# Performance work log

Measured on AMD Instinct MI355X. Metric: run time of the kernel, lower is better.

## Reference

```python
import jax, jax.numpy as jnp
import numpy as np

B, D, K, P = 512, 2048, 128, 5

def setup_inputs() -> dict:
    key = jax.random.key(0)
    k1, k2 = jax.random.split(key)
    x = jax.random.normal(k1, (B, D), dtype=jnp.float32)
    theta = 0.05 * jax.random.normal(k2, (D, K, P), dtype=jnp.float32)
    log_weight_scale = jnp.zeros((K, P), dtype=jnp.float32)
    bias = -jnp.ones((K,), dtype=jnp.float32)  # layer inits bias to -1
    return {"x": x, "theta": theta, "log_weight_scale": log_weight_scale, "bias": bias}

def reference(x, theta, log_weight_scale, bias):
    b = x.shape[0]
    # weight-normalized kernel: [D, K, P]
    norm = jnp.sqrt(jnp.sum(theta * theta, axis=0))            # [K, P]
    kernel = theta * (jnp.exp(log_weight_scale) / norm)[None]  # [D, K, P]
    actv = jnp.einsum('bd,dkp->bkp', x, kernel)                # [B, K, P]
    # pairwise L1 over P: [B, K, B]
    diff = jnp.abs(actv[:, :, :, None] - jnp.transpose(actv, (1, 2, 0))[None])  # [B,K,P,B]
    abs_dif = jnp.sum(diff, axis=2) + 1e6 * jnp.eye(b, dtype=x.dtype)[:, None, :]
    f = jnp.sum(jnp.exp(-abs_dif), axis=2) + bias[None, :]     # [B, K]
    return jnp.concatenate([x, f], axis=1)                     # [B, D+K]
```

## Files before the change

kernel.cpp:

```cpp
#include <hip/hip_runtime.h>
#include <math.h>

#define BSZ 512
#define DD 2048
#define KK 128
#define PP 5
#define NCOL (KK * PP)
#define OUTW (DD + KK)
#define LOG2E 1.4426950408889634f

#define KSPLIT 8
#define GK (DD / KSPLIT)
#define QSPLIT 8

typedef __attribute__((ext_vector_type(8))) short bf16x8;
typedef __attribute__((ext_vector_type(4))) float f32x4;

#define WS_NORM 0
#define WS_ACTV (WS_NORM + NCOL)
#define WS_FPART (WS_ACTV + BSZ * NCOL)
#define WS_XB (WS_FPART + QSPLIT * KK * BSZ)
#define WS_THT (WS_XB + BSZ * DD / 2)
#define WS_PART (WS_THT + NCOL * DD / 2)

__device__ inline ushort f2b(float f) {
    unsigned u = __float_as_uint(f);
    u += 0x7FFF + ((u >> 16) & 1);
    return (ushort)(u >> 16);
}

__global__ __launch_bounds__(256) void prep_kernel(const float* __restrict__ theta,
                                                   const float* __restrict__ x,
                                                   float* __restrict__ norm,
                                                   ushort* __restrict__ thT,
                                                   ushort* __restrict__ xb) {
    __shared__ float partial[32][8];
    __shared__ ushort sT[64][68];

    const int bid = blockIdx.x;
    const int t   = threadIdx.x;

    if (bid < 80) {
        const int c8  = bid * 8;
        const int col = c8 + (t & 7);
        const int g   = t >> 3;
        const float* p = theta + (size_t)g * NCOL + col;
        float s = 0.f;
#pragma unroll
        for (int j = 0; j < 64; ++j) {
            float v = p[(size_t)j * 32 * NCOL];
            s += v * v;
        }
        partial[g][t & 7] = s;
        __syncthreads();
        if (t < 8) {
            float acc = 0.f;
#pragma unroll
            for (int gg = 0; gg < 32; ++gg) acc += partial[gg][t];
            norm[c8 + t] = acc;
        }
    } else if (bid < 400) {
        const int tb    = bid - 80;
        const int kz    = (tb & 31) * 64;
        const int nz    = (tb >> 5) * 64;
        const int c4    = t & 15;
        const int rbase = t >> 4;
#pragma unroll
        for (int i = 0; i < 4; ++i) {
            int r = rbase + i * 16;
            float4 v = *(const float4*)&theta[(size_t)(kz + r) * NCOL + nz + c4 * 4];
            sT[c4 * 4 + 0][r] = f2b(v.x);
            sT[c4 * 4 + 1][r] = f2b(v.y);
            sT[c4 * 4 + 2][r] = f2b(v.z);
            sT[c4 * 4 + 3][r] = f2b(v.w);
        }
        __syncthreads();
#pragma unroll
        for (int i = 0; i < 2; ++i) {
            int slot = t + i * 256;
            int rr   = slot >> 3;
            int cc   = (slot & 7) * 8;
            ushort4 w0 = *(const ushort4*)&sT[rr][cc];
            ushort4 w1 = *(const ushort4*)&sT[rr][cc + 4];
            ushort* dst = &thT[(size_t)(nz + rr) * DD + kz + cc];
            *(ushort4*)&dst[0] = w0;
            *(ushort4*)&dst[4] = w1;
        }
    } else {
        const int b2 = bid - 400;
#pragma unroll
        for (int i = 0; i < 4; ++i) {
            int base = b2 * 4096 + i * 1024 + t * 4;
            float4 v = *(const float4*)&x[base];
            ushort4 w;
            w.x = f2b(v.x); w.y = f2b(v.y); w.z = f2b(v.z); w.w = f2b(v.w);
            *(ushort4*)&xb[base] = w;
        }
    }
}

__global__ __launch_bounds__(256) void gemm_kernel(const ushort* __restrict__ xb,
                                                   const ushort* __restrict__ thT,
                                                   float* __restrict__ part,
                                                   const float* __restrict__ x,
                                                   float* __restrict__ out) {
    __shared__ ushort lA[64][136];
    __shared__ ushort lB[64][136];

    if (blockIdx.z == KSPLIT) {
        const int bid = blockIdx.y * 10 + blockIdx.x;
        for (int i = bid * 256 + threadIdx.x; i < BSZ * (DD / 4); i += 80 * 256) {
            int r = i >> 9;
            int c = i & 511;
            float4 v = *(const float4*)&x[(size_t)r * DD + c * 4];
            *(float4*)&out[(size_t)r * OUTW + c * 4] = v;
        }
        return;
    }

    const int t    = threadIdx.x;
    const int lane = t & 63;
    const int wave = t >> 6;
    const int bn   = blockIdx.x * 64;
    const int bm   = blockIdx.y * 64;
    const int kz   = blockIdx.z * GK;

    const ushort* gA = xb  + (size_t)bm * DD + kz;
    const ushort* gB = thT + (size_t)bn * DD + kz;

    f32x4 acc[2][2] = {};

    uint4 va[4], vb[4];
#pragma unroll
    for (int i = 0; i < 4; ++i) {
        int slot = t + i * 256, rr = slot >> 4, ss = slot & 15;
        va[i] = *(const uint4*)&gA[(size_t)rr * DD + ss * 8];
        vb[i] = *(const uint4*)&gB[(size_t)rr * DD + ss * 8];
    }

    const int fr = lane & 15;
    const int g  = lane >> 4;
    const int mr = (wave >> 1) * 32 + fr;
    const int nr = (wave & 1) * 32 + fr;

#pragma unroll
    for (int c = 0; c < 2; ++c) {
        __syncthreads();
#pragma unroll
        for (int i = 0; i < 4; ++i) {
            int slot = t + i * 256, rr = slot >> 4, ss = slot & 15;
            *(uint4*)&lA[rr][ss * 8] = va[i];
            *(uint4*)&lB[rr][ss * 8] = vb[i];
        }
        __syncthreads();
        if (c == 0) {
#pragma unroll
            for (int i = 0; i < 4; ++i) {
                int slot = t + i * 256, rr = slot >> 4, ss = slot & 15;
                va[i] = *(const uint4*)&gA[(size_t)rr * DD + 128 + ss * 8];
                vb[i] = *(const uint4*)&gB[(size_t)rr * DD + 128 + ss * 8];
            }
        }
#pragma unroll
        for (int ks = 0; ks < 4; ++ks) {
            const int kc = ks * 32 + g * 8;
            bf16x8 a0 = *(const bf16x8*)&lA[mr][kc];
            bf16x8 a1 = *(const bf16x8*)&lA[mr + 16][kc];
            bf16x8 b0 = *(const bf16x8*)&lB[nr][kc];
            bf16x8 b1 = *(const bf16x8*)&lB[nr + 16][kc];
            acc[0][0] = __builtin_amdgcn_mfma_f32_16x16x32_bf16(a0, b0, acc[0][0], 0, 0, 0);
            acc[0][1] = __builtin_amdgcn_mfma_f32_16x16x32_bf16(a0, b1, acc[0][1], 0, 0, 0);
            acc[1][0] = __builtin_amdgcn_mfma_f32_16x16x32_bf16(a1, b0, acc[1][0], 0, 0, 0);
            acc[1][1] = __builtin_amdgcn_mfma_f32_16x16x32_bf16(a1, b1, acc[1][1], 0, 0, 0);
        }
    }

    float* base = part + (size_t)blockIdx.z * (BSZ * NCOL);
#pragma unroll
    for (int mt = 0; mt < 2; ++mt)
#pragma unroll
        for (int nt = 0; nt < 2; ++nt) {
            int row = bm + (wave >> 1) * 32 + mt * 16 + g * 4;
            int col = bn + (wave & 1) * 32 + nt * 16 + fr;
            float* dst = base + (size_t)row * NCOL + col;
#pragma unroll
            for (int reg = 0; reg < 4; ++reg)
                dst[(size_t)reg * NCOL] = acc[mt][nt][reg];
        }
}

__global__ __launch_bounds__(256) void reduce_kernel(const float* __restrict__ part,
                                                     const float* __restrict__ norm,
                                                     const float* __restrict__ lws,
                                                     float* __restrict__ actv) {
    int i   = blockIdx.x * 256 + threadIdx.x;
    int col = i % NCOL;
    float s = 0.f;
#pragma unroll
    for (int q = 0; q < KSPLIT; ++q)
        s += part[(size_t)q * (BSZ * NCOL) + i];
    const float scale = __builtin_amdgcn_exp2f(lws[col] * LOG2E) *
                        __builtin_amdgcn_rsqf(norm[col]) * LOG2E;
    actv[i] = s * scale;
}

__global__ __launch_bounds__(256) void pairwise_kernel(const float* __restrict__ actv,
                                                       float* __restrict__ f_part) {
    const int k   = blockIdx.x;
    const int q   = blockIdx.y;
    const int tid = threadIdx.x;

    __shared__ float sB[64][8];

    for (int i = tid; i < 64 * PP; i += 256) {
        int r = i / PP;
        int p = i - r * PP;
        sB[r][p] = actv[(size_t)(q * 64 + r) * NCOL + k * PP + p];
    }

    float a[2][PP];
#pragma unroll
    for (int r = 0; r < 2; ++r) {
        const float* ap = &actv[(size_t)(tid + r * 256) * NCOL + k * PP];
#pragma unroll
        for (int p = 0; p < PP; ++p) a[r][p] = ap[p];
    }
    __syncthreads();

    float acc[2] = {0.f, 0.f};
#pragma unroll 4
    for (int j = 0; j < 64; ++j) {
        const float4 v  = *(const float4*)&sB[j][0];
        const float  v4 = sB[j][4];
#pragma unroll
        for (int r = 0; r < 2; ++r) {
            float s = fabsf(a[r][0] - v.x) + fabsf(a[r][1] - v.y) +
                      fabsf(a[r][2] - v.z) + fabsf(a[r][3] - v.w) +
                      fabsf(a[r][4] - v4);
            acc[r] += __builtin_amdgcn_exp2f(-s);
        }
    }

    float* fp = f_part + ((size_t)q * KK + k) * BSZ;
    fp[tid]       = acc[0];
    fp[tid + 256] = acc[1];
}

__global__ __launch_bounds__(256) void freduce_kernel(const float* __restrict__ f_part,
                                                      const float* __restrict__ bias,
                                                      float* __restrict__ out) {
    int i = blockIdx.x * 256 + threadIdx.x;
    int k = i >> 9;
    int b = i & 511;
    float s = 0.f;
#pragma unroll
    for (int q = 0; q < QSPLIT; ++q)
        s += f_part[((size_t)q * KK + k) * BSZ + b];
    out[(size_t)b * OUTW + DD + k] = s - 1.0f + bias[k];
}

extern "C" void kernel_launch(void* const* d_in, const int* in_sizes, int n_in,
                              void* d_out, int out_size, void* d_ws, size_t ws_size,
                              hipStream_t stream) {
    const float* x     = (const float*)d_in[0];
    const float* theta = (const float*)d_in[1];
    const float* lws   = (const float*)d_in[2];
    const float* bias  = (const float*)d_in[3];
    float* out = (float*)d_out;

    float* ws     = (float*)d_ws;
    float* norm   = ws + WS_NORM;
    float* actv   = ws + WS_ACTV;
    float* f_part = ws + WS_FPART;
    ushort* xb    = (ushort*)(ws + WS_XB);
    ushort* thT   = (ushort*)(ws + WS_THT);
    float* part   = ws + WS_PART;

    prep_kernel<<<656, 256, 0, stream>>>(theta, x, norm, thT, xb);
    gemm_kernel<<<dim3(NCOL / 64, BSZ / 64, KSPLIT + 1), 256, 0, stream>>>(xb, thT, part, x, out);
    reduce_kernel<<<(BSZ * NCOL) / 256, 256, 0, stream>>>(part, norm, lws, actv);
    pairwise_kernel<<<dim3(KK, QSPLIT), 256, 0, stream>>>(actv, f_part);
    freduce_kernel<<<256, 256, 0, stream>>>(f_part, bias, out);
}
```

Before: 117.8 us.

## Drop split-K in GEMM, fuse scaling epilogue, swizzle LDS tiles

The GEMM no longer splits K eight ways. Each of 80 blocks now loops over the full K=2048 in 16 chunks and writes the scaled activations directly, so the partial-sum buffer and the separate reduce kernel go away. The LDS tiles switch from padded rows to an XOR-swizzled layout to avoid bank conflicts. This saves a launch and the large partial read/write traffic, but leaves only 80 GEMM blocks on a many-CU GPU, each with a longer serial K loop, which may underutilize the device.

```diff
diff --git a/kernel.cpp b/kernel.cpp
--- a/kernel.cpp
+++ b/kernel.cpp
@@ -9,8 +9,6 @@
 #define OUTW (DD + KK)
 #define LOG2E 1.4426950408889634f
 
-#define KSPLIT 8
-#define GK (DD / KSPLIT)
 #define QSPLIT 8
 
 typedef __attribute__((ext_vector_type(8))) short bf16x8;
@@ -21,13 +19,14 @@
 #define WS_FPART (WS_ACTV + BSZ * NCOL)
 #define WS_XB (WS_FPART + QSPLIT * KK * BSZ)
 #define WS_THT (WS_XB + BSZ * DD / 2)
-#define WS_PART (WS_THT + NCOL * DD / 2)
 
 __device__ inline ushort f2b(float f) {
     unsigned u = __float_as_uint(f);
     u += 0x7FFF + ((u >> 16) & 1);
     return (ushort)(u >> 16);
 }
+
+#define SWZ(r, c) ((((r) * 128) + ((c) ^ (((r) & 7) << 3))))
 
 __global__ __launch_bounds__(256) void prep_kernel(const float* __restrict__ theta,
                                                    const float* __restrict__ x,
@@ -101,14 +100,17 @@
 
 __global__ __launch_bounds__(256) void gemm_kernel(const ushort* __restrict__ xb,
                                                    const ushort* __restrict__ thT,
-                                                   float* __restrict__ part,
+                                                   const float* __restrict__ norm,
+                                                   const float* __restrict__ lws,
+                                                   float* __restrict__ actv,
                                                    const float* __restrict__ x,
                                                    float* __restrict__ out) {
-    __shared__ ushort lA[64][136];
-    __shared__ ushort lB[64][136];
-
-    if (blockIdx.z == KSPLIT) {
-        const int bid = blockIdx.y * 10 + blockIdx.x;
+    __shared__ ushort lA[64 * 128];
+    __shared__ ushort lB[64 * 128];
+
+    const int bx = blockIdx.x;
+    if (bx >= 80) {
+        const int bid = bx - 80;
         for (int i = bid * 256 + threadIdx.x; i < BSZ * (DD / 4); i += 80 * 256) {
             int r = i >> 9;
             int c = i & 511;
@@ -121,21 +123,23 @@
     const int t    = threadIdx.x;
     const int lane = t & 63;
     const int wave = t >> 6;
-    const int bn   = blockIdx.x * 64;
-    const int bm   = blockIdx.y * 64;
-    const int kz   = blockIdx.z * GK;
-
-    const ushort* gA = xb  + (size_t)bm * DD + kz;
-    const ushort* gB = thT + (size_t)bn * DD + kz;
+    const int bn   = (bx % 10) * 64;
+    const int bm   = (bx / 10) * 64;
+
+    const ushort* gA = xb  + (size_t)bm * DD;
+    const ushort* gB = thT + (size_t)bn * DD;
 
     f32x4 acc[2][2] = {};
 
+    const int srr = t >> 4;
+    const int sss = t & 15;
+
     uint4 va[4], vb[4];
 #pragma unroll
     for (int i = 0; i < 4; ++i) {
-        int slot = t + i * 256, rr = slot >> 4, ss = slot & 15;
-        va[i] = *(const uint4*)&gA[(size_t)rr * DD + ss * 8];
-        vb[i] = *(const uint4*)&gB[(size_t)rr * DD + ss * 8];
+        int rr = srr + i * 16;
+        va[i] = *(const uint4*)&gA[(size_t)rr * DD + sss * 8];
+        vb[i] = *(const uint4*)&gB[(size_t)rr * DD + sss * 8];
     }
 
     const int fr = lane & 15;
@@ -143,31 +147,31 @@
     const int mr = (wave >> 1) * 32 + fr;
     const int nr = (wave & 1) * 32 + fr;
 
-#pragma unroll
-    for (int c = 0; c < 2; ++c) {
+    for (int c = 0; c < 16; ++c) {
         __syncthreads();
 #pragma unroll
         for (int i = 0; i < 4; ++i) {
-            int slot = t + i * 256, rr = slot >> 4, ss = slot & 15;
-            *(uint4*)&lA[rr][ss * 8] = va[i];
-            *(uint4*)&lB[rr][ss * 8] = vb[i];
-        }
-        __syncthreads();
-        if (c == 0) {
+            int rr = srr + i * 16;
+            *(uint4*)&lA[SWZ(rr, sss * 8)] = va[i];
+            *(uint4*)&lB[SWZ(rr, sss * 8)] = vb[i];
+        }
+        __syncthreads();
+        if (c != 15) {
+            const int kn = (c + 1) * 128;
 #pragma unroll
             for (int i = 0; i < 4; ++i) {
-                int slot = t + i * 256, rr = slot >> 4, ss = slot & 15;
-                va[i] = *(const uint4*)&gA[(size_t)rr * DD + 128 + ss * 8];
-                vb[i] = *(const uint4*)&gB[(size_t)rr * DD + 128 + ss * 8];
+                int rr = srr + i * 16;
+                va[i] = *(const uint4*)&gA[(size_t)rr * DD + kn + sss * 8];
+                vb[i] = *(const uint4*)&gB[(size_t)rr * DD + kn + sss * 8];
             }
         }
 #pragma unroll
         for (int ks = 0; ks < 4; ++ks) {
             const int kc = ks * 32 + g * 8;
-            bf16x8 a0 = *(const bf16x8*)&lA[mr][kc];
-            bf16x8 a1 = *(const bf16x8*)&lA[mr + 16][kc];
-            bf16x8 b0 = *(const bf16x8*)&lB[nr][kc];
-            bf16x8 b1 = *(const bf16x8*)&lB[nr + 16][kc];
+            bf16x8 a0 = *(const bf16x8*)&lA[SWZ(mr,      kc)];
+            bf16x8 a1 = *(const bf16x8*)&lA[SWZ(mr + 16, kc)];
+            bf16x8 b0 = *(const bf16x8*)&lB[SWZ(nr,      kc)];
+            bf16x8 b1 = *(const bf16x8*)&lB[SWZ(nr + 16, kc)];
             acc[0][0] = __builtin_amdgcn_mfma_f32_16x16x32_bf16(a0, b0, acc[0][0], 0, 0, 0);
             acc[0][1] = __builtin_amdgcn_mfma_f32_16x16x32_bf16(a0, b1, acc[0][1], 0, 0, 0);
             acc[1][0] = __builtin_amdgcn_mfma_f32_16x16x32_bf16(a1, b0, acc[1][0], 0, 0, 0);
@@ -175,33 +179,24 @@
         }
     }
 
-    float* base = part + (size_t)blockIdx.z * (BSZ * NCOL);
+    float sc[2];
+#pragma unroll
+    for (int nt = 0; nt < 2; ++nt) {
+        int col = bn + (wave & 1) * 32 + nt * 16 + fr;
+        sc[nt] = __builtin_amdgcn_exp2f(lws[col] * LOG2E) *
+                 __builtin_amdgcn_rsqf(norm[col]) * LOG2E;
+    }
 #pragma unroll
     for (int mt = 0; mt < 2; ++mt)
 #pragma unroll
         for (int nt = 0; nt < 2; ++nt) {
             int row = bm + (wave >> 1) * 32 + mt * 16 + g * 4;
             int col = bn + (wave & 1) * 32 + nt * 16 + fr;
-            float* dst = base + (size_t)row * NCOL + col;
+            float* dst = actv + (size_t)row * NCOL + col;
 #pragma unroll
             for (int reg = 0; reg < 4; ++reg)
-                dst[(size_t)reg * NCOL] = acc[mt][nt][reg];
-        }
-}
-
-__global__ __launch_bounds__(256) void reduce_kernel(const float* __restrict__ part,
-                                                     const float* __restrict__ norm,
-                                                     const float* __restrict__ lws,
-                                                     float* __restrict__ actv) {
-    int i   = blockIdx.x * 256 + threadIdx.x;
-    int col = i % NCOL;
-    float s = 0.f;
-#pragma unroll
-    for (int q = 0; q < KSPLIT; ++q)
-        s += part[(size_t)q * (BSZ * NCOL) + i];
-    const float scale = __builtin_amdgcn_exp2f(lws[col] * LOG2E) *
-                        __builtin_amdgcn_rsqf(norm[col]) * LOG2E;
-    actv[i] = s * scale;
+                dst[(size_t)reg * NCOL] = acc[mt][nt][reg] * sc[nt];
+        }
 }
 
 __global__ __launch_bounds__(256) void pairwise_kernel(const float* __restrict__ actv,
@@ -274,11 +269,9 @@
     float* f_part = ws + WS_FPART;
     ushort* xb    = (ushort*)(ws + WS_XB);
     ushort* thT   = (ushort*)(ws + WS_THT);
-    float* part   = ws + WS_PART;
 
     prep_kernel<<<656, 256, 0, stream>>>(theta, x, norm, thT, xb);
-    gemm_kernel<<<dim3(NCOL / 64, BSZ / 64, KSPLIT + 1), 256, 0, stream>>>(xb, thT, part, x, out);
-    reduce_kernel<<<(BSZ * NCOL) / 256, 256, 0, stream>>>(part, norm, lws, actv);
+    gemm_kernel<<<160, 256, 0, stream>>>(xb, thT, norm, lws, actv, x, out);
     pairwise_kernel<<<dim3(KK, QSPLIT), 256, 0, stream>>>(actv, f_part);
     freduce_kernel<<<256, 256, 0, stream>>>(f_part, bias, out);
 }
```

After: 128.6 us. 1.09x slower.
